# Kernel optimization log

Measured on AMD Instinct MI355X. Metric: run time of the kernel, lower is better.

The kernel has to match this reference:

```python
import jax, jax.numpy as jnp
import numpy as np

EPS = 1e-5

def layer_norm(x, g, b):
    m = x.mean(-1, keepdims=True)
    v = ((x - m) ** 2).mean(-1, keepdims=True)
    return (x - m) * jax.lax.rsqrt(v + EPS) * g + b

def setup_inputs() -> dict:
    key = jax.random.key(0)
    ks = jax.random.split(key, 8)
    H, T = 512, 256
    hidden_states = jax.random.normal(ks[0], (1, T, H), jnp.float32)
    U = jax.random.normal(ks[1], (H, H), jnp.float32) * 0.01
    W = jax.random.normal(ks[2], (H, H), jnp.float32) * 0.01
    a = jax.random.normal(ks[3], (H,), jnp.float32) * 0.01
    b = jax.random.normal(ks[4], (H,), jnp.float32) * 0.01
    gamma = jnp.ones((H,), jnp.float32)
    beta = jnp.zeros((H,), jnp.float32)
    targets = jax.random.randint(ks[5], (T,), 0, H)  # deterministic stand-in for torch.randint dummy targets
    return {"hidden_states": hidden_states, "U": U, "W": W, "a": a, "b": b,
            "gamma": gamma, "beta": beta, "targets": targets}

def reference(hidden_states, U, W, a, b, gamma, beta, targets):
    # batch must be 1 (torch.outer in the original requires 1-D vectors)
    h = hidden_states[0]                      # (T, H)
    z = jax.nn.relu(h @ U + a)                # (T, H) slow-path hidden

    # Per-timestep grads of CE(LayerNorm(z_t @ W + b), target_t) w.r.t. W, b
    def step_loss(z_t, tgt, W_, b_):
        y = layer_norm(z_t @ W_ + b_, gamma, beta)
        return -jax.nn.log_softmax(y)[tgt]
    grad_fn = jax.grad(step_loss, argnums=(2, 3))
    gradW, gradb = jax.vmap(grad_fn, in_axes=(0, 0, None, None))(z, targets, W, b)  # (T,H,H), (T,H)

    # W_update_t[p,q] = sum_{i<t} h_i[p] * h_t[q] * gradW_i[p,q]
    G = h[:, :, None] * gradW                 # (T, H, H)
    A = jnp.cumsum(G, axis=0) - G             # exclusive prefix sum over i
    W_upd = A * h[:, None, :]                 # (T, H, H)
    fastW = W - jnp.cumsum(W_upd, axis=0)     # cumulative fast weights per t

    # b_update_t[q] = h_t[q] * sum_{i<t} (sum_p h_i[p]) * gradb_i[q]
    c = h.sum(-1)                             # (T,)
    Bc = c[:, None] * gradb                   # (T, H)
    Bex = jnp.cumsum(Bc, axis=0) - Bc         # exclusive
    b_upd = h * Bex
    fastb = b - jnp.cumsum(b_upd, axis=0)     # (T, H)

    pre = jnp.einsum('th,thq->tq', z, fastW) + fastb
    out = layer_norm(pre, gamma, beta)        # (T, H)
    return out[None]                          # (1, T, H)
```

## Files before the change

### kernel.cpp

```cpp
#include <hip/hip_runtime.h>

#define T 256
#define H 512
#define EPSF 1e-5f

__device__ __forceinline__ float block_sum(float v, float* s4) {
    for (int o = 32; o; o >>= 1) v += __shfl_xor(v, o);
    int w = threadIdx.x >> 6;
    __syncthreads();
    if ((threadIdx.x & 63) == 0) s4[w] = v;
    __syncthreads();
    return s4[0] + s4[1] + s4[2] + s4[3];
}

__device__ __forceinline__ float block_max(float v, float* s4) {
    for (int o = 32; o; o >>= 1) v = fmaxf(v, __shfl_xor(v, o));
    int w = threadIdx.x >> 6;
    __syncthreads();
    if ((threadIdx.x & 63) == 0) s4[w] = v;
    __syncthreads();
    return fmaxf(fmaxf(s4[0], s4[1]), fmaxf(s4[2], s4[3]));
}

__device__ __forceinline__ float bsum16(float v, float* s16) {
    for (int o = 32; o; o >>= 1) v += __shfl_xor(v, o);
    int w = threadIdx.x >> 6;
    __syncthreads();
    if ((threadIdx.x & 63) == 0) s16[w] = v;
    __syncthreads();
    float r = 0.f;
    #pragma unroll
    for (int i = 0; i < 16; ++i) r += s16[i];
    return r;
}

__global__ __launch_bounds__(256) void k1(
        const float* __restrict__ h, const float* __restrict__ U,
        const float* __restrict__ a, float* __restrict__ Z,
        float* __restrict__ HZ, float* __restrict__ c, float* __restrict__ S) {
    int bid = blockIdx.x, tid = threadIdx.x;
    int lane = tid & 63, w = tid >> 6;
    if (bid < 8) {
        __shared__ float csum[4][64];
        int q = bid * 64 + lane;
        int tbase = w * 64;
        float s = 0.f;
        for (int j = 0; j < 64; j += 8) {
            float v[8];
            #pragma unroll
            for (int u = 0; u < 8; ++u) v[u] = h[(tbase + j + u) * H + q];
            #pragma unroll
            for (int u = 0; u < 8; ++u) s += v[u];
        }
        csum[w][lane] = s;
        __syncthreads();
        float acc = 0.f;
        #pragma unroll
        for (int w2 = 0; w2 < 3; ++w2) if (w2 < w) acc += csum[w2][lane];
        for (int j = 0; j < 64; j += 8) {
            float v[8];
            #pragma unroll
            for (int u = 0; u < 8; ++u) v[u] = h[(tbase + j + u) * H + q];
            #pragma unroll
            for (int u = 0; u < 8; ++u) { acc += v[u]; S[(tbase + j + u) * H + q] = acc; }
        }
        return;
    }
    int b = bid - 8;
    int t0 = (b >> 2) * 2, qt = b & 3;
    __shared__ __align__(16) float sh[1024];
    __shared__ float2 part[3][2][64];
    ((float4*)sh)[tid] = ((const float4*)(h + t0 * H))[tid];
    __syncthreads();

    if (qt == 0 && w < 2) {
        float s = 0.f;
        #pragma unroll
        for (int j = 0; j < 8; ++j) s += sh[w * 512 + lane + j * 64];
        for (int o = 32; o; o >>= 1) s += __shfl_xor(s, o);
        if (lane == 0) c[t0 + w] = s;
    }

    int qc = qt * 64 + lane;
    const float2* U2 = (const float2*)U;
    float2 acc0 = {0.f, 0.f}, acc1 = {0.f, 0.f};
    int kbeg = w * 128;
    for (int k0 = kbeg; k0 < kbeg + 128; k0 += 8) {
        float2 bv[8];
        #pragma unroll
        for (int u = 0; u < 8; ++u) bv[u] = U2[(k0 + u) * 256 + qc];
        float a0[8], a1[8];
        #pragma unroll
        for (int u = 0; u < 8; ++u) { a0[u] = sh[k0 + u]; a1[u] = sh[512 + k0 + u]; }
        #pragma unroll
        for (int u = 0; u < 8; ++u) {
            acc0.x += a0[u] * bv[u].x; acc0.y += a0[u] * bv[u].y;
            acc1.x += a1[u] * bv[u].x; acc1.y += a1[u] * bv[u].y;
        }
    }
    if (w) { part[w - 1][0][lane] = acc0; part[w - 1][1][lane] = acc1; }
    __syncthreads();
    if (w == 0) {
        #pragma unroll
        for (int p = 0; p < 3; ++p) {
            acc0.x += part[p][0][lane].x; acc0.y += part[p][0][lane].y;
            acc1.x += part[p][1][lane].x; acc1.y += part[p][1][lane].y;
        }
        float2 av = ((const float2*)a)[qc];
        float z0x = fmaxf(acc0.x + av.x, 0.f), z0y = fmaxf(acc0.y + av.y, 0.f);
        float z1x = fmaxf(acc1.x + av.x, 0.f), z1y = fmaxf(acc1.y + av.y, 0.f);
        float2 h0 = ((float2*)sh)[qc], h1 = ((float2*)sh)[256 + qc];
        ((float2*)Z)[t0 * 256 + qc]        = make_float2(z0x, z0y);
        ((float2*)Z)[(t0 + 1) * 256 + qc]  = make_float2(z1x, z1y);
        ((float2*)HZ)[t0 * 256 + qc]       = make_float2(h0.x * z0x, h0.y * z0y);
        ((float2*)HZ)[(t0 + 1) * 256 + qc] = make_float2(h1.x * z1x, h1.y * z1y);
    }
}

__global__ __launch_bounds__(256) void k2(
        const float* __restrict__ Z, const float* __restrict__ W,
        const float* __restrict__ bb, const float* __restrict__ HZ,
        const float* __restrict__ c, float* __restrict__ u0,
        float* __restrict__ Beta) {
    __shared__ __align__(16) float smem[2 * 8 * 516 + 256];
    int bid = blockIdx.x, tid = threadIdx.x;
    int lane = tid & 63, w = tid >> 6;
    if (bid < 512) {
        float* sh = smem;
        float2* part = (float2*)(smem + 1024);
        int t0 = (bid >> 2) * 2, qt = bid & 3;
        ((float4*)sh)[tid] = ((const float4*)(Z + t0 * H))[tid];
        __syncthreads();
        int qc = qt * 64 + lane;
        const float2* W2 = (const float2*)W;
        float2 acc0 = {0.f, 0.f}, acc1 = {0.f, 0.f};
        int kbeg = w * 128;
        for (int k0 = kbeg; k0 < kbeg + 128; k0 += 8) {
            float2 bv[8];
            #pragma unroll
            for (int u = 0; u < 8; ++u) bv[u] = W2[(k0 + u) * 256 + qc];
            float a0[8], a1[8];
            #pragma unroll
            for (int u = 0; u < 8; ++u) { a0[u] = sh[k0 + u]; a1[u] = sh[512 + k0 + u]; }
            #pragma unroll
            for (int u = 0; u < 8; ++u) {
                acc0.x += a0[u] * bv[u].x; acc0.y += a0[u] * bv[u].y;
                acc1.x += a1[u] * bv[u].x; acc1.y += a1[u] * bv[u].y;
            }
        }
        if (w) { part[((w - 1) * 2 + 0) * 64 + lane] = acc0; part[((w - 1) * 2 + 1) * 64 + lane] = acc1; }
        __syncthreads();
        if (w == 0) {
            #pragma unroll
            for (int p = 0; p < 3; ++p) {
                float2 p0 = part[(p * 2 + 0) * 64 + lane];
                float2 p1 = part[(p * 2 + 1) * 64 + lane];
                acc0.x += p0.x; acc0.y += p0.y;
                acc1.x += p1.x; acc1.y += p1.y;
            }
            float2 bv = ((const float2*)bb)[qc];
            ((float2*)u0)[t0 * 256 + qc]       = make_float2(acc0.x + bv.x, acc0.y + bv.y);
            ((float2*)u0)[(t0 + 1) * 256 + qc] = make_float2(acc1.x + bv.x, acc1.y + bv.y);
        }
    } else {
        int e = bid - 512;
        int ti = (int)((sqrtf(8.f * (float)e + 1.f) - 1.f) * 0.5f);
        while ((ti + 1) * (ti + 2) / 2 <= e) ++ti;
        while (ti * (ti + 1) / 2 > e) --ti;
        int ii = e - ti * (ti + 1) / 2;
        int t0 = ti * 8, i0 = ii * 8;
        float* Zs = smem;
        float* Hs = smem + 8 * 516;
        float* red = smem + 2 * 8 * 516;
        #pragma unroll
        for (int j = 0; j < 4; ++j) {
            int idx = tid + j * 256;
            int row = idx >> 7, col4 = idx & 127;
            float4 v = ((const float4*)(Z + (t0 + row) * H))[col4];
            *(float4*)&Zs[row * 516 + col4 * 4] = v;
            float4 g = ((const float4*)(HZ + (i0 + row) * H))[col4];
            *(float4*)&Hs[row * 516 + col4 * 4] = g;
        }
        __syncthreads();
        int ks = tid >> 6, r = (tid >> 3) & 7, ci = tid & 7;
        float acc = 0.f;
        int kb = ks * 128;
        #pragma unroll 4
        for (int k0 = kb; k0 < kb + 128; k0 += 8) {
            float4 z0 = *(float4*)&Zs[r * 516 + k0];
            float4 z1 = *(float4*)&Zs[r * 516 + k0 + 4];
            float4 h0 = *(float4*)&Hs[ci * 516 + k0];
            float4 h1 = *(float4*)&Hs[ci * 516 + k0 + 4];
            acc += z0.x * h0.x + z0.y * h0.y + z0.z * h0.z + z0.w * h0.w
                 + z1.x * h1.x + z1.y * h1.y + z1.z * h1.z + z1.w * h1.w;
        }
        red[ks * 64 + r * 8 + ci] = acc;
        __syncthreads();
        if (tid < 64) {
            int r2 = tid >> 3, c2 = tid & 7;
            float v = red[tid] + red[64 + tid] + red[128 + tid] + red[192 + tid];
            int t = t0 + r2, i = i0 + c2;
            Beta[t * 256 + i] = (i < t) ? v + c[i] : 0.f;
        }
    }
}

__global__ __launch_bounds__(256) void k3(
        const float* __restrict__ u0, const float* __restrict__ gamma,
        const float* __restrict__ beta, const int* __restrict__ targets,
        const float* __restrict__ S, float* __restrict__ D, float* __restrict__ SD) {
    __shared__ float s4[4];
    int t = blockIdx.x, tid = threadIdx.x;
    float2 uv = ((const float2*)u0)[t * 256 + tid];
    float2 gv = ((const float2*)gamma)[tid];
    float2 bv = ((const float2*)beta)[tid];

    float m = block_sum(uv.x + uv.y, s4) * (1.f / H);
    float d0 = uv.x - m, d1 = uv.y - m;
    float var = block_sum(d0 * d0 + d1 * d1, s4) * (1.f / H);
    float s = rsqrtf(var + EPSF);
    float xh0 = d0 * s, xh1 = d1 * s;
    float y0 = xh0 * gv.x + bv.x;
    float y1 = xh1 * gv.y + bv.y;

    float ymax = block_max(fmaxf(y0, y1), s4);
    float e0 = __expf(y0 - ymax), e1 = __expf(y1 - ymax);
    float Zs = block_sum(e0 + e1, s4);
    float invZ = 1.f / Zs;
    int tgt = targets[t];
    float g0 = e0 * invZ - (2 * tid == tgt ? 1.f : 0.f);
    float g1 = e1 * invZ - (2 * tid + 1 == tgt ? 1.f : 0.f);
    float gy0 = g0 * gv.x, gy1 = g1 * gv.y;

    float mgy = block_sum(gy0 + gy1, s4) * (1.f / H);
    float mgx = block_sum(gy0 * xh0 + gy1 * xh1, s4) * (1.f / H);

    float dd0 = s * (gy0 - mgy - xh0 * mgx);
    float dd1 = s * (gy1 - mgy - xh1 * mgx);
    float2 sv = ((const float2*)S)[t * 256 + tid];
    ((float2*)D)[t * 256 + tid]  = make_float2(dd0, dd1);
    ((float2*)SD)[t * 256 + tid] = make_float2(sv.x * dd0, sv.y * dd1);
}

__global__ __launch_bounds__(1024) void k4(
        const float* __restrict__ Beta, const float* __restrict__ D,
        const float* __restrict__ SD, const float* __restrict__ u0,
        const float* __restrict__ S, const float* __restrict__ gamma,
        const float* __restrict__ beta, float* __restrict__ out) {
    __shared__ float Brow[256];
    __shared__ float r1[4][512];
    __shared__ float r2[4][512];
    __shared__ float s16[16];
    int t = blockIdx.x, tid = threadIdx.x;
    if (tid < 256) Brow[tid] = Beta[t * 256 + tid];
    __syncthreads();

    int ig = tid >> 8, qc = tid & 255;
    int ibeg = ig * 64;
    int iend = min((t + 7) & ~7, ibeg + 64);
    float2 a1 = {0.f, 0.f}, a2 = {0.f, 0.f};
    const float2* D2 = (const float2*)D;
    const float2* SD2 = (const float2*)SD;
    for (int k0 = ibeg; k0 < iend; k0 += 8) {
        float2 dv[8], sv[8];
        #pragma unroll
        for (int u = 0; u < 8; ++u) {
            dv[u] = D2[(k0 + u) * 256 + qc];
            sv[u] = SD2[(k0 + u) * 256 + qc];
        }
        #pragma unroll
        for (int u = 0; u < 8; ++u) {
            float bw = Brow[k0 + u];
            a1.x += bw * dv[u].x; a1.y += bw * dv[u].y;
            a2.x += bw * sv[u].x; a2.y += bw * sv[u].y;
        }
    }
    r1[ig][2 * qc] = a1.x; r1[ig][2 * qc + 1] = a1.y;
    r2[ig][2 * qc] = a2.x; r2[ig][2 * qc + 1] = a2.y;
    __syncthreads();

    float p = 0.f;
    if (tid < 512) {
        float A1 = r1[0][tid] + r1[1][tid] + r1[2][tid] + r1[3][tid];
        float A2 = r2[0][tid] + r2[1][tid] + r2[2][tid] + r2[3][tid];
        p = u0[t * H + tid] - S[t * H + tid] * A1 + A2;
    }
    float m = bsum16(p, s16) * (1.f / H);
    float d = (tid < 512) ? p - m : 0.f;
    float var = bsum16(d * d, s16) * (1.f / H);
    float s = rsqrtf(var + EPSF);
    if (tid < 512)
        out[t * H + tid] = d * s * gamma[tid] + beta[tid];
}

extern "C" void kernel_launch(void* const* d_in, const int* in_sizes, int n_in,
                              void* d_out, int out_size, void* d_ws, size_t ws_size,
                              hipStream_t stream) {
    const float* h     = (const float*)d_in[0];
    const float* U     = (const float*)d_in[1];
    const float* W     = (const float*)d_in[2];
    const float* a     = (const float*)d_in[3];
    const float* b     = (const float*)d_in[4];
    const float* gamma = (const float*)d_in[5];
    const float* beta  = (const float*)d_in[6];
    const int*   tgt   = (const int*)d_in[7];
    float* out = (float*)d_out;

    float* ws = (float*)d_ws;
    const int TH = T * H;
    float* Z    = ws;
    float* HZ   = Z    + TH;
    float* u0   = HZ   + TH;
    float* D    = u0   + TH;
    float* SD   = D    + TH;
    float* S    = SD   + TH;
    float* c    = S    + TH;
    float* Beta = c    + T;

    k1<<<520,  256, 0, stream>>>(h, U, a, Z, HZ, c, S);
    k2<<<1040, 256, 0, stream>>>(Z, W, b, HZ, c, u0, Beta);
    k3<<<T,    256, 0, stream>>>(u0, gamma, beta, tgt, S, D, SD);
    k4<<<T,   1024, 0, stream>>>(Beta, D, SD, u0, S, gamma, beta, out);
}
```

Before: 112.8 us.

## Process four timesteps per block in k4 to reuse D/SD loads

k4 now handles four consecutive timesteps per block, loading four Beta rows and accumulating four sets of partial sums from each D/SD tile it reads. The aim is to cut the repeated global reads of D and SD, which every timestep previously loaded on its own. The cost is a grid of only 64 blocks, which can leave many compute units idle, plus more registers per thread, serialized per-row layer-norm epilogues and extra barriers.

```diff
diff --git a/kernel.cpp b/kernel.cpp
--- a/kernel.cpp
+++ b/kernel.cpp
@@ -247,18 +247,24 @@
         const float* __restrict__ SD, const float* __restrict__ u0,
         const float* __restrict__ S, const float* __restrict__ gamma,
         const float* __restrict__ beta, float* __restrict__ out) {
-    __shared__ float Brow[256];
+    __shared__ float Brow[4][256];
     __shared__ float r1[4][512];
     __shared__ float r2[4][512];
     __shared__ float s16[16];
-    int t = blockIdx.x, tid = threadIdx.x;
-    if (tid < 256) Brow[tid] = Beta[t * 256 + tid];
+    int t0 = blockIdx.x * 4, tid = threadIdx.x;
+    {
+        int r = tid >> 8, ci = tid & 255;
+        Brow[r][ci] = Beta[(t0 + r) * 256 + ci];
+    }
     __syncthreads();
 
     int ig = tid >> 8, qc = tid & 255;
     int ibeg = ig * 64;
-    int iend = min((t + 7) & ~7, ibeg + 64);
-    float2 a1 = {0.f, 0.f}, a2 = {0.f, 0.f};
+    int ie = min(256, (t0 + 3 + 7) & ~7);
+    int iend = min(ie, ibeg + 64);
+    float2 a1[4], a2[4];
+    #pragma unroll
+    for (int r = 0; r < 4; ++r) { a1[r] = make_float2(0.f, 0.f); a2[r] = make_float2(0.f, 0.f); }
     const float2* D2 = (const float2*)D;
     const float2* SD2 = (const float2*)SD;
     for (int k0 = ibeg; k0 < iend; k0 += 8) {
@@ -270,27 +276,35 @@
         }
         #pragma unroll
         for (int u = 0; u < 8; ++u) {
-            float bw = Brow[k0 + u];
-            a1.x += bw * dv[u].x; a1.y += bw * dv[u].y;
-            a2.x += bw * sv[u].x; a2.y += bw * sv[u].y;
-        }
-    }
-    r1[ig][2 * qc] = a1.x; r1[ig][2 * qc + 1] = a1.y;
-    r2[ig][2 * qc] = a2.x; r2[ig][2 * qc + 1] = a2.y;
-    __syncthreads();
-
-    float p = 0.f;
-    if (tid < 512) {
-        float A1 = r1[0][tid] + r1[1][tid] + r1[2][tid] + r1[3][tid];
-        float A2 = r2[0][tid] + r2[1][tid] + r2[2][tid] + r2[3][tid];
-        p = u0[t * H + tid] - S[t * H + tid] * A1 + A2;
-    }
-    float m = bsum16(p, s16) * (1.f / H);
-    float d = (tid < 512) ? p - m : 0.f;
-    float var = bsum16(d * d, s16) * (1.f / H);
-    float s = rsqrtf(var + EPSF);
-    if (tid < 512)
-        out[t * H + tid] = d * s * gamma[tid] + beta[tid];
+            #pragma unroll
+            for (int r = 0; r < 4; ++r) {
+                float bw = Brow[r][k0 + u];
+                a1[r].x += bw * dv[u].x; a1[r].y += bw * dv[u].y;
+                a2[r].x += bw * sv[u].x; a2[r].y += bw * sv[u].y;
+            }
+        }
+    }
+
+    #pragma unroll
+    for (int r = 0; r < 4; ++r) {
+        r1[ig][2 * qc] = a1[r].x; r1[ig][2 * qc + 1] = a1[r].y;
+        r2[ig][2 * qc] = a2[r].x; r2[ig][2 * qc + 1] = a2[r].y;
+        __syncthreads();
+        float p = 0.f;
+        int t = t0 + r;
+        if (tid < 512) {
+            float A1 = r1[0][tid] + r1[1][tid] + r1[2][tid] + r1[3][tid];
+            float A2 = r2[0][tid] + r2[1][tid] + r2[2][tid] + r2[3][tid];
+            p = u0[t * H + tid] - S[t * H + tid] * A1 + A2;
+        }
+        float m = bsum16(p, s16) * (1.f / H);
+        float d = (tid < 512) ? p - m : 0.f;
+        float var = bsum16(d * d, s16) * (1.f / H);
+        float s = rsqrtf(var + EPSF);
+        if (tid < 512)
+            out[t * H + tid] = d * s * gamma[tid] + beta[tid];
+        __syncthreads();
+    }
 }
 
 extern "C" void kernel_launch(void* const* d_in, const int* in_sizes, int n_in,
@@ -317,8 +331,8 @@
     float* c    = S    + TH;
     float* Beta = c    + T;
 
-    k1<<<520,  256, 0, stream>>>(h, U, a, Z, HZ, c, S);
-    k2<<<1040, 256, 0, stream>>>(Z, W, b, HZ, c, u0, Beta);
-    k3<<<T,    256, 0, stream>>>(u0, gamma, beta, tgt, S, D, SD);
-    k4<<<T,   1024, 0, stream>>>(Beta, D, SD, u0, S, gamma, beta, out);
-}
+    k1<<<520,    256, 0, stream>>>(h, U, a, Z, HZ, c, S);
+    k2<<<1040,   256, 0, stream>>>(Z, W, b, HZ, c, u0, Beta);
+    k3<<<T,      256, 0, stream>>>(u0, gamma, beta, tgt, S, D, SD);
+    k4<<<T / 4, 1024, 0, stream>>>(Beta, D, SD, u0, S, gamma, beta, out);
+}
```

Result: slower. 119.4 us (+5.8%).

## Split final stage into row-tiled prefix matmul and separate LayerNorm kernel

Applied to the files above, without the earlier changes.

Replaces the per-timestep 1024-thread k4 with k4a, where each block handles 8 consecutive timesteps and a 32-column slice. Each loaded D/SD row is reused across the 8 timestep rows, so global traffic on D/SD drops roughly eightfold. Partial sums are reduced in shared memory and written to a new pre buffer. A separate k4b then applies LayerNorm per row. The cost is an extra launch plus a write and read of the pre buffer, and inner-loop register pressure goes up.

```diff
diff --git a/kernel.cpp b/kernel.cpp
--- a/kernel.cpp
+++ b/kernel.cpp
@@ -20,18 +20,6 @@
     if ((threadIdx.x & 63) == 0) s4[w] = v;
     __syncthreads();
     return fmaxf(fmaxf(s4[0], s4[1]), fmaxf(s4[2], s4[3]));
-}
-
-__device__ __forceinline__ float bsum16(float v, float* s16) {
-    for (int o = 32; o; o >>= 1) v += __shfl_xor(v, o);
-    int w = threadIdx.x >> 6;
-    __syncthreads();
-    if ((threadIdx.x & 63) == 0) s16[w] = v;
-    __syncthreads();
-    float r = 0.f;
-    #pragma unroll
-    for (int i = 0; i < 16; ++i) r += s16[i];
-    return r;
 }
 
 __global__ __launch_bounds__(256) void k1(
@@ -242,55 +230,87 @@
     ((float2*)SD)[t * 256 + tid] = make_float2(sv.x * dd0, sv.y * dd1);
 }
 
-__global__ __launch_bounds__(1024) void k4(
+__global__ __launch_bounds__(256) void k4a(
         const float* __restrict__ Beta, const float* __restrict__ D,
         const float* __restrict__ SD, const float* __restrict__ u0,
-        const float* __restrict__ S, const float* __restrict__ gamma,
-        const float* __restrict__ beta, float* __restrict__ out) {
-    __shared__ float Brow[256];
-    __shared__ float r1[4][512];
-    __shared__ float r2[4][512];
-    __shared__ float s16[16];
-    int t = blockIdx.x, tid = threadIdx.x;
-    if (tid < 256) Brow[tid] = Beta[t * 256 + tid];
-    __syncthreads();
-
-    int ig = tid >> 8, qc = tid & 255;
-    int ibeg = ig * 64;
-    int iend = min((t + 7) & ~7, ibeg + 64);
-    float2 a1 = {0.f, 0.f}, a2 = {0.f, 0.f};
+        const float* __restrict__ S, float* __restrict__ pre) {
+    __shared__ float Brow[8][256];
+    __shared__ float2 red1[8][8][32];
+    __shared__ float2 red2[8][8][32];
+    int bid = blockIdx.x, tid = threadIdx.x;
+    int R0 = (bid >> 3) * 8;
+    int g  = bid & 7;
+    #pragma unroll
+    for (int j = 0; j < 8; ++j) {
+        int idx = tid + j * 256;
+        int r = idx >> 8, ci = idx & 255;
+        Brow[r][ci] = Beta[(R0 + r) * 256 + ci];
+    }
+    __syncthreads();
+
+    int ks = tid >> 5, cc = tid & 31;
+    int qc = g * 32 + cc;
+    int kend = R0 + 8;
+    float2 a1[8], a2[8];
+    #pragma unroll
+    for (int r = 0; r < 8; ++r) { a1[r] = make_float2(0.f, 0.f); a2[r] = make_float2(0.f, 0.f); }
     const float2* D2 = (const float2*)D;
     const float2* SD2 = (const float2*)SD;
-    for (int k0 = ibeg; k0 < iend; k0 += 8) {
+    for (int i0 = ks * 8; i0 < kend; i0 += 64) {
         float2 dv[8], sv[8];
         #pragma unroll
         for (int u = 0; u < 8; ++u) {
-            dv[u] = D2[(k0 + u) * 256 + qc];
-            sv[u] = SD2[(k0 + u) * 256 + qc];
+            dv[u] = D2[(i0 + u) * 256 + qc];
+            sv[u] = SD2[(i0 + u) * 256 + qc];
         }
         #pragma unroll
         for (int u = 0; u < 8; ++u) {
-            float bw = Brow[k0 + u];
-            a1.x += bw * dv[u].x; a1.y += bw * dv[u].y;
-            a2.x += bw * sv[u].x; a2.y += bw * sv[u].y;
-        }
-    }
-    r1[ig][2 * qc] = a1.x; r1[ig][2 * qc + 1] = a1.y;
-    r2[ig][2 * qc] = a2.x; r2[ig][2 * qc + 1] = a2.y;
-    __syncthreads();
-
-    float p = 0.f;
-    if (tid < 512) {
-        float A1 = r1[0][tid] + r1[1][tid] + r1[2][tid] + r1[3][tid];
-        float A2 = r2[0][tid] + r2[1][tid] + r2[2][tid] + r2[3][tid];
-        p = u0[t * H + tid] - S[t * H + tid] * A1 + A2;
-    }
-    float m = bsum16(p, s16) * (1.f / H);
-    float d = (tid < 512) ? p - m : 0.f;
-    float var = bsum16(d * d, s16) * (1.f / H);
+            #pragma unroll
+            for (int r = 0; r < 8; ++r) {
+                float bw = Brow[r][i0 + u];
+                a1[r].x += bw * dv[u].x; a1[r].y += bw * dv[u].y;
+                a2[r].x += bw * sv[u].x; a2[r].y += bw * sv[u].y;
+            }
+        }
+    }
+    #pragma unroll
+    for (int r = 0; r < 8; ++r) { red1[ks][r][cc] = a1[r]; red2[ks][r][cc] = a2[r]; }
+    __syncthreads();
+
+    {
+        int r = tid >> 5, c = tid & 31;
+        float2 A1 = make_float2(0.f, 0.f), A2 = make_float2(0.f, 0.f);
+        #pragma unroll
+        for (int p = 0; p < 8; ++p) {
+            float2 v1 = red1[p][r][c], v2 = red2[p][r][c];
+            A1.x += v1.x; A1.y += v1.y;
+            A2.x += v2.x; A2.y += v2.y;
+        }
+        int t = R0 + r;
+        int col = g * 32 + c;
+        float2 uv = ((const float2*)u0)[t * 256 + col];
+        float2 sv = ((const float2*)S)[t * 256 + col];
+        float2 p;
+        p.x = uv.x - sv.x * A1.x + A2.x;
+        p.y = uv.y - sv.y * A1.y + A2.y;
+        ((float2*)pre)[t * 256 + col] = p;
+    }
+}
+
+__global__ __launch_bounds__(256) void k4b(
+        const float* __restrict__ pre, const float* __restrict__ gamma,
+        const float* __restrict__ beta, float* __restrict__ out) {
+    __shared__ float s4[4];
+    int t = blockIdx.x, tid = threadIdx.x;
+    float2 pv = ((const float2*)pre)[t * 256 + tid];
+    float m = block_sum(pv.x + pv.y, s4) * (1.f / H);
+    float d0 = pv.x - m, d1 = pv.y - m;
+    float var = block_sum(d0 * d0 + d1 * d1, s4) * (1.f / H);
     float s = rsqrtf(var + EPSF);
-    if (tid < 512)
-        out[t * H + tid] = d * s * gamma[tid] + beta[tid];
+    float2 gv = ((const float2*)gamma)[tid];
+    float2 bv = ((const float2*)beta)[tid];
+    ((float2*)out)[t * 256 + tid] =
+        make_float2(d0 * s * gv.x + bv.x, d1 * s * gv.y + bv.y);
 }
 
 extern "C" void kernel_launch(void* const* d_in, const int* in_sizes, int n_in,
@@ -316,9 +336,11 @@
     float* S    = SD   + TH;
     float* c    = S    + TH;
     float* Beta = c    + T;
+    float* pre  = Beta + T * T;
 
     k1<<<520,  256, 0, stream>>>(h, U, a, Z, HZ, c, S);
     k2<<<1040, 256, 0, stream>>>(Z, W, b, HZ, c, u0, Beta);
     k3<<<T,    256, 0, stream>>>(u0, gamma, beta, tgt, S, D, SD);
-    k4<<<T,   1024, 0, stream>>>(Beta, D, SD, u0, S, gamma, beta, out);
-}
+    k4a<<<256, 256, 0, stream>>>(Beta, D, SD, u0, S, pre);
+    k4b<<<T,   256, 0, stream>>>(pre, gamma, beta, out);
+}
```

Measured after the change: 104.3 us. -7.6%, faster.
